# Performance work log

Hardware: AMD Instinct MI355X
Metric: run time of the kernel (lower is better)

The kernel has to match this reference:

```python
import jax, jax.numpy as jnp
import numpy as np


def bilinear_sample(img, xs, ys):
    # img: [C,H,W]; xs, ys: [Ho,Wo] fractional source coords (pixel units).
    # Zero-fill outside the image, matching grid_sample(padding_mode='zeros').
    C, H, W = img.shape
    x0f = jnp.floor(xs); y0f = jnp.floor(ys)
    wx = xs - x0f; wy = ys - y0f
    x0 = x0f.astype(jnp.int32); y0 = y0f.astype(jnp.int32)

    def gather(yi, xi):
        inb = ((xi >= 0) & (xi <= W - 1) & (yi >= 0) & (yi <= H - 1))
        xc = jnp.clip(xi, 0, W - 1); yc = jnp.clip(yi, 0, H - 1)
        return img[:, yc, xc] * inb[None].astype(img.dtype)

    v00 = gather(y0,     x0)
    v01 = gather(y0,     x0 + 1)
    v10 = gather(y0 + 1, x0)
    v11 = gather(y0 + 1, x0 + 1)
    return (v00 * (1 - wx) * (1 - wy) + v01 * wx * (1 - wy)
            + v10 * (1 - wx) * wy + v11 * wx * wy)


def setup_inputs() -> dict:
    key = jax.random.key(0)
    k1, k2 = jax.random.split(key)
    frame = jax.random.uniform(k1, (1, 4, 1080, 1920), dtype=jnp.float32)
    # last channel is the alpha/transparency mask: fully opaque frame
    frame = frame.at[:, -1].set(1.0)
    canvas = jax.random.uniform(k2, (1, 4, 2048, 3072), dtype=jnp.float32)
    # realistic near-identity homography: small rotation + translation + tiny perspective
    th = 0.02
    Hmat = jnp.array([[np.cos(th), -np.sin(th), 400.0],
                      [np.sin(th),  np.cos(th), 300.0],
                      [1e-6,        0.0,        1.0]], dtype=jnp.float32)
    return {"frame": frame, "Hmat": Hmat, "canvas": canvas}


def reference(frame, Hmat, canvas):
    # Homography warp of `frame` into the canvas coordinate grid (inverse warp +
    # bilinear resample), then 'over' alpha-compositing onto the canvas
    # (merge_frame), fused into one pass over the canvas buffer.
    _, C, Hc, Wc = canvas.shape
    Hinv = jnp.linalg.inv(Hmat)
    dt = frame.dtype
    ys, xs = jnp.meshgrid(jnp.arange(Hc, dtype=dt), jnp.arange(Wc, dtype=dt), indexing='ij')
    coords = jnp.stack([xs, ys, jnp.ones_like(xs)])          # [3,Hc,Wc]
    src = jnp.einsum('ij,jhw->ihw', Hinv, coords)            # [3,Hc,Wc]
    sx = src[0] / src[2]
    sy = src[1] / src[2]
    warped = bilinear_sample(frame[0], sx, sy)               # [C,Hc,Wc]
    a_s = warped[-1:]                                        # source alpha
    a_c = canvas[0, -1:]                                     # canvas alpha
    out_rgb = warped[:-1] * a_s + canvas[0, :-1] * a_c * (1.0 - a_s)
    out_a = a_s + a_c * (1.0 - a_s)
    return jnp.concatenate([out_rgb, out_a], axis=0)[None]   # [1,C,Hc,Wc]
```

## Files before the change

kernel.cpp:

```cpp
#include <hip/hip_runtime.h>


#define FH 1080
#define FW 1920
#define CH 2048
#define CW 3072
#define FHW (FH * FW)
#define CHW (CH * CW)

__global__ __launch_bounds__(256) void pano_kernel(
    const float* __restrict__ frame,
    const float* __restrict__ Hm,
    const float* __restrict__ canvas,
    float* __restrict__ out)
{
    const int x = blockIdx.x * 256 + threadIdx.x;
    const int y = blockIdx.y;
    const int pix = y * CW + x;

    const float a  = Hm[0], b  = Hm[1], c  = Hm[2];
    const float d  = Hm[3], e  = Hm[4], f  = Hm[5];
    const float g  = Hm[6], hh = Hm[7], i9 = Hm[8];

    const float A0 = e * i9 - f * hh, A1 = c * hh - b * i9, A2 = b * f - c * e;
    const float B0 = f * g  - d * i9, B1 = a * i9 - c * g,  B2 = c * d - a * f;
    const float C0 = d * hh - e * g,  C1 = b * g  - a * hh, C2 = a * e - b * d;

    const float xf = (float)x, yf = (float)y;
    const float u = A0 * xf + A1 * yf + A2;
    const float v = B0 * xf + B1 * yf + B2;
    const float w = C0 * xf + C1 * yf + C2;
    const float sx = u / w;
    const float sy = v / w;

    const float x0f = floorf(sx);
    const float y0f = floorf(sy);
    const float wx = sx - x0f;
    const float wy = sy - y0f;
    const int x0 = (int)x0f;
    const int y0 = (int)y0f;

    const float c0 = canvas[0 * CHW + pix];
    const float c1 = canvas[1 * CHW + pix];
    const float c2 = canvas[2 * CHW + pix];
    const float ac = canvas[3 * CHW + pix];

    float w0 = 0.f, w1 = 0.f, w2 = 0.f, as = 0.f;

    if (x0 >= -1 && x0 <= FW - 1 && y0 >= -1 && y0 <= FH - 1) {
        const int x1 = x0 + 1, y1 = y0 + 1;
        const float mx0 = (x0 >= 0 && x0 <= FW - 1) ? 1.f : 0.f;
        const float mx1 = (x1 >= 0 && x1 <= FW - 1) ? 1.f : 0.f;
        const float my0 = (y0 >= 0 && y0 <= FH - 1) ? 1.f : 0.f;
        const float my1 = (y1 >= 0 && y1 <= FH - 1) ? 1.f : 0.f;
        const int xc0 = min(max(x0, 0), FW - 1);
        const int xc1 = min(max(x1, 0), FW - 1);
        const int yc0 = min(max(y0, 0), FH - 1);
        const int yc1 = min(max(y1, 0), FH - 1);

        const float w00 = (1.f - wx) * (1.f - wy) * mx0 * my0;
        const float w01 = wx * (1.f - wy) * mx1 * my0;
        const float w10 = (1.f - wx) * wy * mx0 * my1;
        const float w11 = wx * wy * mx1 * my1;

        const int i00 = yc0 * FW + xc0;
        const int i01 = yc0 * FW + xc1;
        const int i10 = yc1 * FW + xc0;
        const int i11 = yc1 * FW + xc1;

        #pragma unroll
        for (int ch = 0; ch < 4; ++ch) {
            const float* fp = frame + ch * FHW;
            const float val = w00 * fp[i00] + w01 * fp[i01]
                            + w10 * fp[i10] + w11 * fp[i11];
            if (ch == 0) w0 = val;
            else if (ch == 1) w1 = val;
            else if (ch == 2) w2 = val;
            else as = val;
        }
    }

    const float k = ac * (1.f - as);
    out[0 * CHW + pix] = w0 * as + c0 * k;
    out[1 * CHW + pix] = w1 * as + c1 * k;
    out[2 * CHW + pix] = w2 * as + c2 * k;
    out[3 * CHW + pix] = as + k;
}

extern "C" void kernel_launch(void* const* d_in, const int* in_sizes, int n_in,
                              void* d_out, int out_size, void* d_ws, size_t ws_size,
                              hipStream_t stream) {
    const float* frame  = (const float*)d_in[0];
    const float* Hm     = (const float*)d_in[1];
    const float* canvas = (const float*)d_in[2];
    float* out = (float*)d_out;

    dim3 block(256, 1, 1);
    dim3 grid(CW / 256, CH, 1);
    pano_kernel<<<grid, block, 0, stream>>>(frame, Hm, canvas, out);
}
```

Baseline: 203.3 us.

## Interleave frame channels into float4 and process four canvas pixels per thread

A pre-pass kernel repacks the planar frame into an interleaved RGBA float4 buffer in workspace, so each bilinear tap becomes one 16-byte gather instead of four scattered scalar loads. The main kernel now handles four consecutive canvas pixels per thread with float4 canvas loads and stores, and replaces the division with a hardware reciprocal. The cost is an extra kernel launch and a full read and write of the frame (about 33 MB each way) every call. The approximate reciprocal may change rounding slightly.

```diff
diff --git a/kernel.cpp b/kernel.cpp
--- a/kernel.cpp
+++ b/kernel.cpp
@@ -3,10 +3,116 @@
 
 #define FH 1080
 #define FW 1920
-#define CH 2048
-#define CW 3072
+#define CHh 2048
+#define CWw 3072
 #define FHW (FH * FW)
-#define CHW (CH * CW)
+#define CHW (CHh * CWw)
+
+__global__ __launch_bounds__(256) void interleave_kernel(
+    const float* __restrict__ frame, float4* __restrict__ fi)
+{
+    const int idx = blockIdx.x * 256 + threadIdx.x;
+    float4 v;
+    v.x = frame[idx];
+    v.y = frame[FHW + idx];
+    v.z = frame[2 * FHW + idx];
+    v.w = frame[3 * FHW + idx];
+    fi[idx] = v;
+}
+
+__global__ __launch_bounds__(256) void pano4_kernel(
+    const float4* __restrict__ fi,
+    const float* __restrict__ Hm,
+    const float* __restrict__ canvas,
+    float* __restrict__ out)
+{
+    const int t = blockIdx.x * 256 + threadIdx.x;
+    const int y = blockIdx.y;
+    const int x4 = t * 4;
+    const int q = y * (CWw / 4) + t;
+
+    const float a  = Hm[0], b  = Hm[1], c  = Hm[2];
+    const float d  = Hm[3], e  = Hm[4], f  = Hm[5];
+    const float g  = Hm[6], hh = Hm[7], i9 = Hm[8];
+    const float A0 = e * i9 - f * hh, A1 = c * hh - b * i9, A2 = b * f - c * e;
+    const float B0 = f * g  - d * i9, B1 = a * i9 - c * g,  B2 = c * d - a * f;
+    const float C0 = d * hh - e * g,  C1 = b * g  - a * hh, C2 = a * e - b * d;
+
+    const float4* cv = (const float4*)canvas;
+    const float4 cr = cv[0 * (CHW / 4) + q];
+    const float4 cg = cv[1 * (CHW / 4) + q];
+    const float4 cb = cv[2 * (CHW / 4) + q];
+    const float4 ca = cv[3 * (CHW / 4) + q];
+
+    float wr[4], wg[4], wb[4], wa[4];
+    const float yf = (float)y;
+
+    #pragma unroll
+    for (int p = 0; p < 4; ++p) {
+        wr[p] = wg[p] = wb[p] = wa[p] = 0.f;
+        const float xf = (float)(x4 + p);
+        const float u = fmaf(A0, xf, fmaf(A1, yf, A2));
+        const float v = fmaf(B0, xf, fmaf(B1, yf, B2));
+        const float w = fmaf(C0, xf, fmaf(C1, yf, C2));
+        const float invw = __builtin_amdgcn_rcpf(w);
+        const float sx = u * invw;
+        const float sy = v * invw;
+        const float x0f = floorf(sx);
+        const float y0f = floorf(sy);
+        const float wx = sx - x0f;
+        const float wy = sy - y0f;
+        const int x0 = (int)x0f;
+        const int y0 = (int)y0f;
+
+        if (x0 >= -1 && x0 <= FW - 1 && y0 >= -1 && y0 <= FH - 1) {
+            const int x1 = x0 + 1, y1 = y0 + 1;
+            const float mx0 = (x0 >= 0) ? 1.f : 0.f;
+            const float mx1 = (x1 <= FW - 1) ? 1.f : 0.f;
+            const float my0 = (y0 >= 0) ? 1.f : 0.f;
+            const float my1 = (y1 <= FH - 1) ? 1.f : 0.f;
+            const int xc0 = min(max(x0, 0), FW - 1);
+            const int xc1 = min(max(x1, 0), FW - 1);
+            const int yc0 = min(max(y0, 0), FH - 1);
+            const int yc1 = min(max(y1, 0), FH - 1);
+
+            const float w00 = (1.f - wx) * (1.f - wy) * mx0 * my0;
+            const float w01 = wx * (1.f - wy) * mx1 * my0;
+            const float w10 = (1.f - wx) * wy * mx0 * my1;
+            const float w11 = wx * wy * mx1 * my1;
+
+            const float4 v00 = fi[yc0 * FW + xc0];
+            const float4 v01 = fi[yc0 * FW + xc1];
+            const float4 v10 = fi[yc1 * FW + xc0];
+            const float4 v11 = fi[yc1 * FW + xc1];
+
+            wr[p] = fmaf(w00, v00.x, fmaf(w01, v01.x, fmaf(w10, v10.x, w11 * v11.x)));
+            wg[p] = fmaf(w00, v00.y, fmaf(w01, v01.y, fmaf(w10, v10.y, w11 * v11.y)));
+            wb[p] = fmaf(w00, v00.z, fmaf(w01, v01.z, fmaf(w10, v10.z, w11 * v11.z)));
+            wa[p] = fmaf(w00, v00.w, fmaf(w01, v01.w, fmaf(w10, v10.w, w11 * v11.w)));
+        }
+    }
+
+    const float crr[4] = {cr.x, cr.y, cr.z, cr.w};
+    const float cgg[4] = {cg.x, cg.y, cg.z, cg.w};
+    const float cbb[4] = {cb.x, cb.y, cb.z, cb.w};
+    const float caa[4] = {ca.x, ca.y, ca.z, ca.w};
+
+    float orv[4], ogv[4], obv[4], oav[4];
+    #pragma unroll
+    for (int p = 0; p < 4; ++p) {
+        const float k = caa[p] * (1.f - wa[p]);
+        orv[p] = fmaf(wr[p], wa[p], crr[p] * k);
+        ogv[p] = fmaf(wg[p], wa[p], cgg[p] * k);
+        obv[p] = fmaf(wb[p], wa[p], cbb[p] * k);
+        oav[p] = wa[p] + k;
+    }
+
+    float4* ov = (float4*)out;
+    ov[0 * (CHW / 4) + q] = make_float4(orv[0], orv[1], orv[2], orv[3]);
+    ov[1 * (CHW / 4) + q] = make_float4(ogv[0], ogv[1], ogv[2], ogv[3]);
+    ov[2 * (CHW / 4) + q] = make_float4(obv[0], obv[1], obv[2], obv[3]);
+    ov[3 * (CHW / 4) + q] = make_float4(oav[0], oav[1], oav[2], oav[3]);
+}
 
 __global__ __launch_bounds__(256) void pano_kernel(
     const float* __restrict__ frame,
@@ -16,12 +122,11 @@
 {
     const int x = blockIdx.x * 256 + threadIdx.x;
     const int y = blockIdx.y;
-    const int pix = y * CW + x;
+    const int pix = y * CWw + x;
 
     const float a  = Hm[0], b  = Hm[1], c  = Hm[2];
     const float d  = Hm[3], e  = Hm[4], f  = Hm[5];
     const float g  = Hm[6], hh = Hm[7], i9 = Hm[8];
-
     const float A0 = e * i9 - f * hh, A1 = c * hh - b * i9, A2 = b * f - c * e;
     const float B0 = f * g  - d * i9, B1 = a * i9 - c * g,  B2 = c * d - a * f;
     const float C0 = d * hh - e * g,  C1 = b * g  - a * hh, C2 = a * e - b * d;
@@ -46,13 +151,12 @@
     const float ac = canvas[3 * CHW + pix];
 
     float w0 = 0.f, w1 = 0.f, w2 = 0.f, as = 0.f;
-
     if (x0 >= -1 && x0 <= FW - 1 && y0 >= -1 && y0 <= FH - 1) {
         const int x1 = x0 + 1, y1 = y0 + 1;
-        const float mx0 = (x0 >= 0 && x0 <= FW - 1) ? 1.f : 0.f;
-        const float mx1 = (x1 >= 0 && x1 <= FW - 1) ? 1.f : 0.f;
-        const float my0 = (y0 >= 0 && y0 <= FH - 1) ? 1.f : 0.f;
-        const float my1 = (y1 >= 0 && y1 <= FH - 1) ? 1.f : 0.f;
+        const float mx0 = (x0 >= 0) ? 1.f : 0.f;
+        const float mx1 = (x1 <= FW - 1) ? 1.f : 0.f;
+        const float my0 = (y0 >= 0) ? 1.f : 0.f;
+        const float my1 = (y1 <= FH - 1) ? 1.f : 0.f;
         const int xc0 = min(max(x0, 0), FW - 1);
         const int xc1 = min(max(x1, 0), FW - 1);
         const int yc0 = min(max(y0, 0), FH - 1);
@@ -69,13 +173,13 @@
         const int i11 = yc1 * FW + xc1;
 
         #pragma unroll
-        for (int ch = 0; ch < 4; ++ch) {
-            const float* fp = frame + ch * FHW;
+        for (int chn = 0; chn < 4; ++chn) {
+            const float* fp = frame + chn * FHW;
             const float val = w00 * fp[i00] + w01 * fp[i01]
                             + w10 * fp[i10] + w11 * fp[i11];
-            if (ch == 0) w0 = val;
-            else if (ch == 1) w1 = val;
-            else if (ch == 2) w2 = val;
+            if (chn == 0) w0 = val;
+            else if (chn == 1) w1 = val;
+            else if (chn == 2) w2 = val;
             else as = val;
         }
     }
@@ -95,7 +199,12 @@
     const float* canvas = (const float*)d_in[2];
     float* out = (float*)d_out;
 
-    dim3 block(256, 1, 1);
-    dim3 grid(CW / 256, CH, 1);
-    pano_kernel<<<grid, block, 0, stream>>>(frame, Hm, canvas, out);
-}
+    const size_t need = (size_t)FHW * sizeof(float4);
+    if (ws_size >= need) {
+        float4* fi = (float4*)d_ws;
+        interleave_kernel<<<dim3(FHW / 256), dim3(256), 0, stream>>>(frame, fi);
+        pano4_kernel<<<dim3(CWw / 4 / 256, CHh), dim3(256), 0, stream>>>(fi, Hm, canvas, out);
+    } else {
+        pano_kernel<<<dim3(CWw / 256, CHh), dim3(256), 0, stream>>>(frame, Hm, canvas, out);
+    }
+}
```

Measured after the change: 225.6 us. 1.11x slower.
